# Kernel optimization log

Hardware: AMD Instinct MI355X
Metric: run time of the kernel (lower is better)

The kernel has to match this reference:

```python
import jax, jax.numpy as jnp
import numpy as np


def setup_inputs() -> dict:
    key = jax.random.key(0)
    k1, k2, k3, k4 = jax.random.split(key, 4)
    T, H, E, I = 4096, 1024, 8, 3584
    return {
        "hidden_states": jax.random.normal(k1, (T, H), dtype=jnp.float32),
        "gate_w": jax.random.normal(k2, (H, E), dtype=jnp.float32) * 0.02,
        "w1": jax.random.normal(k3, (E, H, I), dtype=jnp.float32) * 0.02,
        "w2": jax.random.normal(k4, (E, I, H), dtype=jnp.float32) * 0.02,
        "top_k": 2,
    }


def reference(hidden_states, gate_w, w1, w2, top_k):
    # Router: logits -> softmax -> top-k -> renormalize (Mixtral / vLLM fused_moe)
    router_logits = hidden_states @ gate_w                    # [T, E]
    probs = jax.nn.softmax(router_logits, axis=-1)
    top_vals, top_idx = jax.lax.top_k(probs, top_k)           # [T, K]
    top_vals = top_vals / jnp.sum(top_vals, axis=-1, keepdims=True)
    E = gate_w.shape[1]
    # Dense per-(token, expert) combine weights, zero for non-selected experts
    dense_w = jnp.sum(jax.nn.one_hot(top_idx, E, dtype=hidden_states.dtype)
                      * top_vals[..., None], axis=1)          # [T, E]
    # Expert MLP: silu(x @ w1[e]) @ w2[e], weighted by routing probs
    act = jax.nn.silu(jnp.einsum('th,ehi->tei', hidden_states, w1))  # [T, E, I]
    act = act * dense_w[:, :, None]
    out = jnp.einsum('tei,eih->th', act, w2)                  # [T, H]
    return out
```

## Files before the change

kernel.cpp:

```cpp
#include <hip/hip_runtime.h>
#include <hip/hip_bf16.h>

#define T_TOK 4096
#define H_DIM 1024
#define E_NUM 8
#define I_DIM 3584
#define NPAIR (T_TOK * 2)
#define MAX_RT 72

#define BM 128
#define BN 128
#define BK 64

typedef __attribute__((ext_vector_type(8))) short bf16x8;
typedef __attribute__((ext_vector_type(4))) float f32x4;
typedef __attribute__((ext_vector_type(8))) unsigned short ushort8_t;
typedef __attribute__((ext_vector_type(4))) unsigned short ushort4_t;

__device__ __forceinline__ unsigned short f2bf(float x) {
  unsigned int u = __float_as_uint(x);
  unsigned int r = (u + 0x7FFFu + ((u >> 16) & 1u)) >> 16;
  return (unsigned short)r;
}

__device__ __forceinline__ void gload16(const void* g, unsigned short* l) {
  __builtin_amdgcn_global_load_lds(
      (const __attribute__((address_space(1))) void*)g,
      (__attribute__((address_space(3))) void*)l, 16, 0, 0);
}

__global__ void transpose_cvt(const float* __restrict__ src,
                              unsigned short* __restrict__ dst, int R, int C) {
  __shared__ float tile[64][65];
  const int e = blockIdx.z;
  const int c0 = blockIdx.x * 64, r0 = blockIdx.y * 64;
  const float* s = src + (size_t)e * R * C;
  unsigned short* d = dst + (size_t)e * R * C;
  const int th = threadIdx.x;
  const int tr = th >> 4;
  const int tc4 = (th & 15) * 4;
#pragma unroll
  for (int it = 0; it < 4; ++it) {
    const int r = it * 16 + tr;
    float4 v = *reinterpret_cast<const float4*>(s + (size_t)(r0 + r) * C + c0 + tc4);
    tile[r][tc4] = v.x; tile[r][tc4 + 1] = v.y; tile[r][tc4 + 2] = v.z; tile[r][tc4 + 3] = v.w;
  }
  __syncthreads();
  const int wc = th >> 3;
  const int wr = (th & 7) * 8;
#pragma unroll
  for (int it = 0; it < 2; ++it) {
    const int c = it * 32 + wc;
    ushort8_t o;
#pragma unroll
    for (int j = 0; j < 8; ++j) o[j] = f2bf(tile[wr + j][c]);
    *reinterpret_cast<ushort8_t*>(d + (size_t)(c0 + c) * R + r0 + wr) = o;
  }
}

__global__ void router_kernel(const float* __restrict__ hs, const float* __restrict__ gw,
                              unsigned short* __restrict__ hsb,
                              int* __restrict__ eid, float* __restrict__ wgt,
                              int* __restrict__ counts) {
  __shared__ float s_gw[8192];
  __shared__ int s_cnt[E_NUM];
  const int th = threadIdx.x;
  for (int u = th; u < 2048; u += 256) {
    const f32x4 v = *reinterpret_cast<const f32x4*>(gw + u * 4);
    *reinterpret_cast<f32x4*>(&s_gw[(u ^ ((u >> 3) & 7)) * 4]) = v;
  }
  if (th < E_NUM) s_cnt[th] = 0;
  __syncthreads();

  const int l = th & 63, w = th >> 6;
#pragma unroll 1
  for (int tt = 0; tt < 4; ++tt) {
    const int t = blockIdx.x * 16 + w * 4 + tt;
    const float* hrow = hs + (size_t)t * H_DIM;
    unsigned short* brow = hsb + (size_t)t * H_DIM;
    float acc[E_NUM];
#pragma unroll
    for (int e = 0; e < E_NUM; ++e) acc[e] = 0.f;
#pragma unroll
    for (int i = 0; i < 4; ++i) {
      const int h0 = i * 256 + l * 4;
      const f32x4 x = *reinterpret_cast<const f32x4*>(hrow + h0);
      ushort4_t o = { f2bf(x[0]), f2bf(x[1]), f2bf(x[2]), f2bf(x[3]) };
      *reinterpret_cast<ushort4_t*>(brow + h0) = o;
#pragma unroll
      for (int j = 0; j < 4; ++j) {
        const int h = h0 + j;
        const int p0 = (h * 2) ^ ((h >> 2) & 7);
        const f32x4 g0 = *reinterpret_cast<const f32x4*>(&s_gw[p0 * 4]);
        const f32x4 g1 = *reinterpret_cast<const f32x4*>(&s_gw[(p0 ^ 1) * 4]);
        acc[0] += x[j] * g0[0]; acc[1] += x[j] * g0[1];
        acc[2] += x[j] * g0[2]; acc[3] += x[j] * g0[3];
        acc[4] += x[j] * g1[0]; acc[5] += x[j] * g1[1];
        acc[6] += x[j] * g1[2]; acc[7] += x[j] * g1[3];
      }
    }
#pragma unroll
    for (int e = 0; e < E_NUM; ++e) {
#pragma unroll
      for (int off = 1; off < 64; off <<= 1) acc[e] += __shfl_xor(acc[e], off);
    }
    if (l == 0) {
      int i1 = 0;
#pragma unroll
      for (int e = 1; e < E_NUM; ++e) if (acc[e] > acc[i1]) i1 = e;
      int i2 = (i1 == 0) ? 1 : 0;
#pragma unroll
      for (int e = 0; e < E_NUM; ++e) if (e != i1 && acc[e] > acc[i2]) i2 = e;
      const float e2 = __expf(acc[i2] - acc[i1]);
      const float inv = 1.f / (1.f + e2);
      eid[t * 2] = i1;     wgt[t * 2] = inv;
      eid[t * 2 + 1] = i2; wgt[t * 2 + 1] = e2 * inv;
      atomicAdd(&s_cnt[i1], 1);
      atomicAdd(&s_cnt[i2], 1);
    }
  }
  __syncthreads();
  if (th < E_NUM && s_cnt[th] > 0) atomicAdd(&counts[th], s_cnt[th]);
}

__global__ void scatter_kernel(const int* __restrict__ eid, const int* __restrict__ counts,
                               int* __restrict__ fill, int* __restrict__ rowmap) {
  __shared__ int hist[E_NUM], base[E_NUM];
  const int th = threadIdx.x;
  const int p = blockIdx.x * 256 + th;
  if (th < E_NUM) hist[th] = 0;
  __syncthreads();
  const int e = eid[p];
  const int rloc = atomicAdd(&hist[e], 1);
  __syncthreads();
  if (th < E_NUM) base[th] = (hist[th] > 0) ? atomicAdd(&fill[th], hist[th]) : 0;
  __syncthreads();
  int off = 0;
#pragma unroll
  for (int i = 0; i < E_NUM; ++i) off += (i < e) ? counts[i] : 0;
  rowmap[off + base[e] + rloc] = p;
}

template <int MODE, int NCT>
__launch_bounds__(256, 3)
__global__ void moe_gemm(const unsigned short* __restrict__ hsb,
                         const unsigned short* __restrict__ wt,
                         const unsigned short* __restrict__ act_in,
                         unsigned short* __restrict__ act_out,
                         float* __restrict__ out,
                         const int* __restrict__ counts,
                         const int* __restrict__ rowmap,
                         const float* __restrict__ wgt) {
  constexpr int KD = (MODE == 0) ? H_DIM : I_DIM;
  constexpr int NWG = MAX_RT * NCT;

  __shared__ unsigned short As[BM * BK];
  __shared__ unsigned short Bs[BN * BK];
  __shared__ int s_pair[BM];
  __shared__ float s_w[BM];

  const int bid = blockIdx.x;
  const int wgid = (bid & 7) * (NWG / 8) + (bid >> 3);
  const int rt = wgid / NCT;
  const int ct = wgid % NCT;

  int e = -1, loc_rt = 0, off_e = 0, cnt = 0;
  {
    int acc_t = 0, off = 0;
#pragma unroll
    for (int ee = 0; ee < E_NUM; ++ee) {
      const int c = counts[ee];
      const int nt = (c + BM - 1) >> 7;
      if (e < 0 && rt < acc_t + nt) { e = ee; loc_rt = rt - acc_t; off_e = off; cnt = c; }
      acc_t += nt; off += c;
    }
  }
  if (e < 0) return;

  const int cnt_local = min(BM, cnt - loc_rt * BM);
  const int r_base = off_e + loc_rt * BM;
  const int th = threadIdx.x;
  const int lane = th & 63, wid = th >> 6;

  if (MODE == 1 && th < BM) {
    int r = loc_rt * BM + th;
    if (r >= cnt) r = cnt - 1;
    const int p = rowmap[off_e + r];
    s_pair[th] = p;
    s_w[th] = wgt[p];
  }

  const int n0 = ct * BN;
  const unsigned short* wbase = wt + (size_t)e * ((size_t)I_DIM * H_DIM) + (size_t)n0 * KD;

  const int srow = lane >> 3;
  const int cg = (lane & 7) ^ srow;
  const char* aptr[4];
  const char* bptr[4];
#pragma unroll
  for (int i = 0; i < 4; ++i) {
    const int r = i * 32 + wid * 8 + srow;
    const int rr = (r < cnt_local) ? r : (cnt_local - 1);
    if (MODE == 0) {
      const int tok = rowmap[off_e + loc_rt * BM + rr] >> 1;
      aptr[i] = (const char*)(hsb + (size_t)tok * H_DIM) + cg * 16;
    } else {
      aptr[i] = (const char*)(act_in + (size_t)(r_base + rr) * I_DIM) + cg * 16;
    }
    bptr[i] = (const char*)(wbase + (size_t)r * KD) + cg * 16;
  }
  unsigned short* dstA[4];
  unsigned short* dstB[4];
#pragma unroll
  for (int i = 0; i < 4; ++i) {
    dstA[i] = &As[(i * 32 + wid * 8) * BK];
    dstB[i] = &Bs[(i * 32 + wid * 8) * BK];
  }

  f32x4 acc[4][4];
#pragma unroll
  for (int m = 0; m < 4; ++m)
#pragma unroll
    for (int n = 0; n < 4; ++n) acc[m][n] = (f32x4){0.f, 0.f, 0.f, 0.f};

  const int wm = (wid >> 1) * 64;
  const int wn = (wid & 1) * 64;
  const int fr = lane & 15;
  const int fq = lane >> 4;
  const int sxor = fr & 7;

  for (int k0 = 0; k0 < KD; k0 += BK) {
    const int kb = k0 * 2;
#pragma unroll
    for (int i = 0; i < 4; ++i) gload16(aptr[i] + kb, dstA[i]);
#pragma unroll
    for (int i = 0; i < 4; ++i) gload16(bptr[i] + kb, dstB[i]);
    __syncthreads();

#pragma unroll
    for (int kk = 0; kk < 2; ++kk) {
      bf16x8 af[4], bf[4];
#pragma unroll
      for (int m = 0; m < 4; ++m)
        af[m] = *reinterpret_cast<const bf16x8*>(
            &As[(wm + m * 16 + fr) * BK + ((kk * 4 + fq) ^ sxor) * 8]);
#pragma unroll
      for (int n = 0; n < 4; ++n)
        bf[n] = *reinterpret_cast<const bf16x8*>(
            &Bs[(wn + n * 16 + fr) * BK + ((kk * 4 + fq) ^ sxor) * 8]);
#pragma unroll
      for (int m = 0; m < 4; ++m)
#pragma unroll
        for (int n = 0; n < 4; ++n)
          acc[m][n] = __builtin_amdgcn_mfma_f32_16x16x32_bf16(af[m], bf[n], acc[m][n], 0, 0, 0);
    }
    __syncthreads();
  }

#pragma unroll
  for (int m = 0; m < 4; ++m) {
    const int row = wm + m * 16 + fq * 4;
#pragma unroll
    for (int n = 0; n < 4; ++n) {
      const int col = wn + n * 16 + fr;
#pragma unroll
      for (int r = 0; r < 4; ++r) {
        const int rw = row + r;
        if (rw < cnt_local) {
          const float x = acc[m][n][r];
          if (MODE == 0) {
            const float s = x / (1.f + __expf(-x));
            act_out[(size_t)(r_base + rw) * I_DIM + n0 + col] = f2bf(s);
          } else {
            const int p = s_pair[rw];
            const int tok = p >> 1;
            atomicAdd(out + (size_t)tok * H_DIM + n0 + col, x * s_w[rw]);
          }
        }
      }
    }
  }
}

extern "C" void kernel_launch(void* const* d_in, const int* in_sizes, int n_in,
                              void* d_out, int out_size, void* d_ws, size_t ws_size,
                              hipStream_t stream) {
  const float* hs = (const float*)d_in[0];
  const float* gw = (const float*)d_in[1];
  const float* w1 = (const float*)d_in[2];
  const float* w2 = (const float*)d_in[3];
  float* out = (float*)d_out;

  char* ws = (char*)d_ws;
  const size_t WMAT = (size_t)E_NUM * I_DIM * H_DIM * 2;
  unsigned short* w1t = (unsigned short*)ws;
  unsigned short* w2t = (unsigned short*)(ws + WMAT);
  unsigned short* act = (unsigned short*)(ws + 2 * WMAT);
  unsigned short* hsb = (unsigned short*)(ws + 3 * WMAT);
  char* small = ws + 3 * WMAT + (size_t)T_TOK * H_DIM * 2;
  int* eid = (int*)small;
  float* wgt = (float*)(small + NPAIR * 4);
  int* rowmap = (int*)(small + 2 * NPAIR * 4);
  int* counts = (int*)(small + 3 * NPAIR * 4);
  int* fill = counts + 8;

  hipMemsetAsync(d_out, 0, (size_t)T_TOK * H_DIM * sizeof(float), stream);
  hipMemsetAsync(counts, 0, 16 * sizeof(int), stream);

  transpose_cvt<<<dim3(I_DIM / 64, H_DIM / 64, E_NUM), 256, 0, stream>>>(w1, w1t, H_DIM, I_DIM);
  transpose_cvt<<<dim3(H_DIM / 64, I_DIM / 64, E_NUM), 256, 0, stream>>>(w2, w2t, I_DIM, H_DIM);

  router_kernel<<<T_TOK / 16, 256, 0, stream>>>(hs, gw, hsb, eid, wgt, counts);
  scatter_kernel<<<NPAIR / 256, 256, 0, stream>>>(eid, counts, fill, rowmap);

  moe_gemm<0, I_DIM / BN><<<MAX_RT * (I_DIM / BN), 256, 0, stream>>>(
      hsb, w1t, nullptr, act, nullptr, counts, rowmap, wgt);
  moe_gemm<1, H_DIM / BN><<<MAX_RT * (H_DIM / BN), 256, 0, stream>>>(
      hsb, w2t, act, nullptr, out, counts, rowmap, wgt);
}
```

Before: 286.4 us.

## Replace atomic scatter-add in down-projection with per-pair buffer and combine kernel

```diff
diff --git a/kernel.cpp b/kernel.cpp
--- a/kernel.cpp
+++ b/kernel.cpp
@@ -124,7 +124,8 @@
 }
 
 __global__ void scatter_kernel(const int* __restrict__ eid, const int* __restrict__ counts,
-                               int* __restrict__ fill, int* __restrict__ rowmap) {
+                               int* __restrict__ fill, int* __restrict__ rowmap,
+                               int* __restrict__ posmap) {
   __shared__ int hist[E_NUM], base[E_NUM];
   const int th = threadIdx.x;
   const int p = blockIdx.x * 256 + th;
@@ -138,16 +139,30 @@
   int off = 0;
 #pragma unroll
   for (int i = 0; i < E_NUM; ++i) off += (i < e) ? counts[i] : 0;
-  rowmap[off + base[e] + rloc] = p;
+  const int pos = off + base[e] + rloc;
+  rowmap[pos] = p;
+  posmap[p] = pos;
+}
+
+__global__ void combine_kernel(const float* __restrict__ res, const int* __restrict__ posmap,
+                               float* __restrict__ out) {
+  const int t = blockIdx.x;
+  const int th = threadIdx.x;
+  const int a = posmap[t * 2];
+  const int b = posmap[t * 2 + 1];
+  const float4 va = *reinterpret_cast<const float4*>(res + (size_t)a * H_DIM + th * 4);
+  const float4 vb = *reinterpret_cast<const float4*>(res + (size_t)b * H_DIM + th * 4);
+  float4 o = { va.x + vb.x, va.y + vb.y, va.z + vb.z, va.w + vb.w };
+  *reinterpret_cast<float4*>(out + (size_t)t * H_DIM + th * 4) = o;
 }
 
 template <int MODE, int NCT>
-__launch_bounds__(256, 3)
+__launch_bounds__(256, 4)
 __global__ void moe_gemm(const unsigned short* __restrict__ hsb,
                          const unsigned short* __restrict__ wt,
                          const unsigned short* __restrict__ act_in,
                          unsigned short* __restrict__ act_out,
-                         float* __restrict__ out,
+                         float* __restrict__ res,
                          const int* __restrict__ counts,
                          const int* __restrict__ rowmap,
                          const float* __restrict__ wgt) {
@@ -156,7 +171,6 @@
 
   __shared__ unsigned short As[BM * BK];
   __shared__ unsigned short Bs[BN * BK];
-  __shared__ int s_pair[BM];
   __shared__ float s_w[BM];
 
   const int bid = blockIdx.x;
@@ -185,9 +199,7 @@
   if (MODE == 1 && th < BM) {
     int r = loc_rt * BM + th;
     if (r >= cnt) r = cnt - 1;
-    const int p = rowmap[off_e + r];
-    s_pair[th] = p;
-    s_w[th] = wgt[p];
+    s_w[th] = wgt[rowmap[off_e + r]];
   }
 
   const int n0 = ct * BN;
@@ -272,9 +284,7 @@
             const float s = x / (1.f + __expf(-x));
             act_out[(size_t)(r_base + rw) * I_DIM + n0 + col] = f2bf(s);
           } else {
-            const int p = s_pair[rw];
-            const int tok = p >> 1;
-            atomicAdd(out + (size_t)tok * H_DIM + n0 + col, x * s_w[rw]);
+            res[(size_t)(r_base + rw) * H_DIM + n0 + col] = x * s_w[rw];
           }
         }
       }
@@ -297,24 +307,27 @@
   unsigned short* w2t = (unsigned short*)(ws + WMAT);
   unsigned short* act = (unsigned short*)(ws + 2 * WMAT);
   unsigned short* hsb = (unsigned short*)(ws + 3 * WMAT);
+  float* res = (float*)w1t;
   char* small = ws + 3 * WMAT + (size_t)T_TOK * H_DIM * 2;
   int* eid = (int*)small;
   float* wgt = (float*)(small + NPAIR * 4);
   int* rowmap = (int*)(small + 2 * NPAIR * 4);
-  int* counts = (int*)(small + 3 * NPAIR * 4);
+  int* posmap = (int*)(small + 3 * NPAIR * 4);
+  int* counts = (int*)(small + 4 * NPAIR * 4);
   int* fill = counts + 8;
 
-  hipMemsetAsync(d_out, 0, (size_t)T_TOK * H_DIM * sizeof(float), stream);
   hipMemsetAsync(counts, 0, 16 * sizeof(int), stream);
 
   transpose_cvt<<<dim3(I_DIM / 64, H_DIM / 64, E_NUM), 256, 0, stream>>>(w1, w1t, H_DIM, I_DIM);
   transpose_cvt<<<dim3(H_DIM / 64, I_DIM / 64, E_NUM), 256, 0, stream>>>(w2, w2t, I_DIM, H_DIM);
 
   router_kernel<<<T_TOK / 16, 256, 0, stream>>>(hs, gw, hsb, eid, wgt, counts);
-  scatter_kernel<<<NPAIR / 256, 256, 0, stream>>>(eid, counts, fill, rowmap);
+  scatter_kernel<<<NPAIR / 256, 256, 0, stream>>>(eid, counts, fill, rowmap, posmap);
 
   moe_gemm<0, I_DIM / BN><<<MAX_RT * (I_DIM / BN), 256, 0, stream>>>(
       hsb, w1t, nullptr, act, nullptr, counts, rowmap, wgt);
   moe_gemm<1, H_DIM / BN><<<MAX_RT * (H_DIM / BN), 256, 0, stream>>>(
-      hsb, w2t, act, nullptr, out, counts, rowmap, wgt);
-}
+      hsb, w2t, act, nullptr, res, counts, rowmap, wgt);
+
+  combine_kernel<<<T_TOK, 256, 0, stream>>>(res, posmap, out);
+}
```

Measured after the change: 286.3 us. No clear change (-0.1%).
